# Optimization experiments

Hardware: AMD Instinct MI355X
Metric: run time of the kernel (lower is better)

The kernel has to match this reference:

```python
import jax, jax.numpy as jnp
import numpy as np
import math

D_MODEL = 1024
NUM_HEADS = 16
B, S = 4, 2048


def setup_inputs() -> dict:
    key = jax.random.key(0)
    ks = jax.random.split(key, 12)
    d = D_MODEL
    sc = 1.0 / math.sqrt(d)
    inp = {
        "q": jax.random.normal(ks[0], (B, S, d), jnp.float32),
        "k": jax.random.normal(ks[1], (B, S, d), jnp.float32),
        "v": jax.random.normal(ks[2], (B, S, d), jnp.float32),
        # causal mask, broadcast over batch and heads
        "mask": jnp.tril(jnp.ones((S, S), bool))[None, None, :, :],
        "Wq": jax.random.normal(ks[3], (d, d), jnp.float32) * sc,
        "bq": jnp.zeros((d,), jnp.float32),
        "Wk": jax.random.normal(ks[4], (d, d), jnp.float32) * sc,
        "bk": jnp.zeros((d,), jnp.float32),
        "Wv": jax.random.normal(ks[5], (d, d), jnp.float32) * sc,
        "bv": jnp.zeros((d,), jnp.float32),
        "Wo": jax.random.normal(ks[6], (d, d), jnp.float32) * sc,
        "bo": jnp.zeros((d,), jnp.float32),
    }
    return inp


def reference(q, k, v, mask, Wq, bq, Wk, bk, Wv, bv, Wo, bo):
    b, s, d = q.shape
    h = NUM_HEADS
    dk = d // h
    # QKV projections, then split heads: [B, H, S, dk]
    def split(x):
        return x.reshape(b, -1, h, dk).transpose(0, 2, 1, 3)
    Q = split(q @ Wq + bq)
    K = split(k @ Wk + bk)
    V = split(v @ Wv + bv)
    scores = jnp.einsum("bhqd,bhkd->bhqk", Q, K) / jnp.sqrt(jnp.float32(dk))
    scores = jnp.where(mask, scores, jnp.float32(-jnp.inf))
    attn = jax.nn.softmax(scores, axis=-1)  # dropout is identity in eval
    ctx = jnp.einsum("bhqk,bhkd->bhqd", attn, V)
    ctx = ctx.transpose(0, 2, 1, 3).reshape(b, -1, d)
    return ctx @ Wo + bo
```

## Files before the change

kernel.cpp:

```cpp
#include <hip/hip_runtime.h>
#include <hip/hip_bf16.h>

typedef unsigned short u16;
typedef __bf16 bf16x8 __attribute__((ext_vector_type(8)));
typedef float f32x4 __attribute__((ext_vector_type(4)));

#define D_MODEL 1024
#define NUM_HEADS 16
#define BATCH 4
#define SEQ 2048
#define DK 64
#define MROWS (BATCH * SEQ)
#define TENS (MROWS * D_MODEL)

#define GLOAD16(gp, lp) __builtin_amdgcn_global_load_lds( \
    (const __attribute__((address_space(1))) void*)(gp), \
    (__attribute__((address_space(3))) void*)(lp), 16, 0, 0)

__device__ inline u16 f2bf(float f) {
    __hip_bfloat16 h = __float2bfloat16(f);
    return *reinterpret_cast<u16*>(&h);
}

__global__ __launch_bounds__(256) void transpose4(
    const float* __restrict__ W0, const float* __restrict__ W1,
    const float* __restrict__ W2, const float* __restrict__ W3,
    u16* __restrict__ dst)
{
    __shared__ u16 tile[32][33];
    const float* in = (blockIdx.z == 0) ? W0 : (blockIdx.z == 1) ? W1
                    : (blockIdx.z == 2) ? W2 : W3;
    u16* out = dst + (size_t)blockIdx.z * (D_MODEL * D_MODEL);
    int x = blockIdx.x * 32 + threadIdx.x;
    int y = blockIdx.y * 32 + threadIdx.y;
    for (int i = 0; i < 32; i += 8)
        tile[threadIdx.y + i][threadIdx.x] = f2bf(in[(size_t)(y + i) * D_MODEL + x]);
    __syncthreads();
    x = blockIdx.y * 32 + threadIdx.x;
    y = blockIdx.x * 32 + threadIdx.y;
    for (int i = 0; i < 32; i += 8)
        out[(size_t)(y + i) * D_MODEL + x] = tile[threadIdx.x][threadIdx.y + i];
}

__global__ __launch_bounds__(256) void cvt_bf16(
    const float* __restrict__ x0, const float* __restrict__ x1,
    const float* __restrict__ x2,
    u16* __restrict__ o0, u16* __restrict__ o1, u16* __restrict__ o2)
{
    const int z = blockIdx.z;
    const float* x = (z == 0) ? x0 : (z == 1) ? x1 : x2;
    u16* o = (z == 0) ? o0 : (z == 1) ? o1 : o2;
    size_t i = ((size_t)blockIdx.x * 256 + threadIdx.x) * 8;
    f32x4 a = *(const f32x4*)(x + i);
    f32x4 b = *(const f32x4*)(x + i + 4);
    union { u16 s[8]; uint4 v; } u;
    for (int t = 0; t < 4; t++) { u.s[t] = f2bf(a[t]); u.s[4 + t] = f2bf(b[t]); }
    *(uint4*)(o + i) = u.v;
}

__global__ __launch_bounds__(256) void prep_fused(
    const float* __restrict__ q, const float* __restrict__ k,
    const float* __restrict__ v,
    u16* __restrict__ s0, u16* __restrict__ s1, u16* __restrict__ s2,
    const float* __restrict__ W0, const float* __restrict__ W1,
    const float* __restrict__ W2, const float* __restrict__ W3,
    u16* __restrict__ wt)
{
    __shared__ u16 tile[32][33];
    const int z = blockIdx.z;
    if (z < 3) {
        const float* x = (z == 0) ? q : (z == 1) ? k : v;
        u16* o = (z == 0) ? s0 : (z == 1) ? s1 : s2;
        size_t i = ((size_t)blockIdx.x * 256 + threadIdx.x) * 8;
        f32x4 a = *(const f32x4*)(x + i);
        f32x4 b = *(const f32x4*)(x + i + 4);
        union { u16 s[8]; uint4 v4; } u;
        for (int t = 0; t < 4; t++) { u.s[t] = f2bf(a[t]); u.s[4 + t] = f2bf(b[t]); }
        *(uint4*)(o + i) = u.v4;
    } else {
        const int bx = blockIdx.x & 31;
        const int by = (blockIdx.x >> 5) & 31;
        const int bz = blockIdx.x >> 10;
        const int tx = threadIdx.x & 31;
        const int ty = threadIdx.x >> 5;
        const float* in = (bz == 0) ? W0 : (bz == 1) ? W1
                        : (bz == 2) ? W2 : W3;
        u16* out = wt + (size_t)bz * (D_MODEL * D_MODEL);
        int x = bx * 32 + tx;
        int y = by * 32 + ty;
        for (int i = 0; i < 32; i += 8)
            tile[ty + i][tx] = f2bf(in[(size_t)(y + i) * D_MODEL + x]);
        __syncthreads();
        x = by * 32 + tx;
        y = bx * 32 + ty;
        for (int i = 0; i < 32; i += 8)
            out[(size_t)(y + i) * D_MODEL + x] = tile[tx][ty + i];
    }
}

template<bool C_F32>
__global__ __launch_bounds__(256) void gemm_b(
    const u16* __restrict__ A0, const u16* __restrict__ A1,
    const u16* __restrict__ A2,
    const u16* __restrict__ Bt0, const u16* __restrict__ Bt1,
    const u16* __restrict__ Bt2,
    const float* __restrict__ bias0, const float* __restrict__ bias1,
    const float* __restrict__ bias2,
    void* __restrict__ C0, void* __restrict__ C1, void* __restrict__ C2,
    float os0, float os1, float os2)
{
    const int z = blockIdx.z;
    const u16* A      = (z == 0) ? A0 : (z == 1) ? A1 : A2;
    const u16* Bt     = (z == 0) ? Bt0 : (z == 1) ? Bt1 : Bt2;
    const float* bias = (z == 0) ? bias0 : (z == 1) ? bias1 : bias2;
    void* Cp          = (z == 0) ? C0 : (z == 1) ? C1 : C2;
    const float os    = (z == 0) ? os0 : (z == 1) ? os1 : os2;
    const int K = D_MODEL, N = D_MODEL;

    __shared__ __align__(16) u16 As[128 * 32];
    __shared__ __align__(16) u16 Bs[128 * 32];

    const int tid  = threadIdx.x;
    const int lane = tid & 63;
    const int w    = tid >> 6;
    const int wr   = w >> 1, wc = w & 1;
    const int m0   = blockIdx.x * 128;
    const int n0   = blockIdx.y * 128;
    const int col_l = lane & 15;
    const int quad  = lane >> 4;
    const int koff  = quad * 8;

    const f32x4 fz = {0.f, 0.f, 0.f, 0.f};
    f32x4 acc[4][4];
    for (int i = 0; i < 4; i++)
        for (int j = 0; j < 4; j++) acc[i][j] = fz;

    for (int k0 = 0; k0 < K; k0 += 32) {
        __syncthreads();
        for (int i = 0; i < 2; i++) {
            int c   = w * 2 + i;
            int row = c * 16 + (lane >> 2);
            GLOAD16(A  + (size_t)(m0 + row) * K + k0 + (lane & 3) * 8, (char*)As + c * 1024);
            GLOAD16(Bt + (size_t)(n0 + row) * K + k0 + (lane & 3) * 8, (char*)Bs + c * 1024);
        }
        __syncthreads();

        bf16x8 af[4], bfr[4];
        for (int i = 0; i < 4; i++)
            af[i] = *(const bf16x8*)&As[(wr * 64 + i * 16 + col_l) * 32 + koff];
        for (int j = 0; j < 4; j++)
            bfr[j] = *(const bf16x8*)&Bs[(wc * 64 + j * 16 + col_l) * 32 + koff];
        for (int i = 0; i < 4; i++)
            for (int j = 0; j < 4; j++)
                acc[i][j] = __builtin_amdgcn_mfma_f32_16x16x32_bf16(
                    af[i], bfr[j], acc[i][j], 0, 0, 0);
    }

    const int row_q = quad * 4;
    for (int j = 0; j < 4; j++) {
        int colg = n0 + wc * 64 + j * 16 + col_l;
        float bv = bias[colg];
        for (int i = 0; i < 4; i++) {
            int rowg = m0 + wr * 64 + i * 16 + row_q;
            for (int r = 0; r < 4; r++) {
                float val = (acc[i][j][r] + bv) * os;
                if (C_F32)
                    ((float*)Cp)[(size_t)(rowg + r) * N + colg] = val;
                else
                    ((u16*)Cp)[(size_t)(rowg + r) * N + colg] = f2bf(val);
            }
        }
    }
}

__global__ __launch_bounds__(256) void attn_kernel(
    const u16* __restrict__ Q, const u16* __restrict__ K,
    const u16* __restrict__ V, u16* __restrict__ ctx)
{
    __shared__ __align__(16) u16 Ksf[64 * 64];
    __shared__ __align__(16) u16 Vts[64 * 64];
    __shared__ __align__(16) u16 Ps[4][16][72];

    const int tid  = threadIdx.x;
    const int lane = tid & 63;
    const int w    = tid >> 6;
    const int bh   = blockIdx.x;
    const int iy = blockIdx.y;
    const int sj = iy >> 2, jj4 = iy & 3;
    const int qt = (sj == 0) ? jj4 : (sj == 1) ? 15 - jj4
                 : (sj == 2) ? 7 - jj4 : 8 + jj4;
    const int b    = bh >> 4, h = bh & 15;
    const int q0   = qt * 128;
    const size_t rowbase = (size_t)b * SEQ;
    const int colbase = h * DK;

    const int col_l = lane & 15;
    const int quad  = lane >> 4;
    const int r0 = tid >> 3, cc0 = tid & 7, r1 = r0 + 32;

    const int c0 = w * 2, c1 = c0 + 1;
    const int krow0 = c0 * 8 + (lane >> 3), krow1 = c1 * 8 + (lane >> 3);
    const int bb0 = (lane & 7) ^ (krow0 & 7), bb1 = (lane & 7) ^ (krow1 & 7);
    const u16* Kg0 = K + (rowbase + krow0) * D_MODEL + colbase + bb0 * 8;
    const u16* Kg1 = K + (rowbase + krow1) * D_MODEL + colbase + bb1 * 8;
    u16* KsW0 = &Ksf[c0 * 512 + lane * 8];
    u16* KsW1 = &Ksf[c1 * 512 + lane * 8];
    const u16* Vg0 = V + (rowbase + r0) * D_MODEL + colbase + cc0 * 8;
    const u16* Vg1 = V + (rowbase + r1) * D_MODEL + colbase + cc0 * 8;

    bf16x8 aq[2][2];
    for (int rb = 0; rb < 2; rb++) {
        const u16* qp = Q + (rowbase + q0 + rb * 64 + w * 16 + col_l) * D_MODEL + colbase;
        aq[rb][0] = *(const bf16x8*)(qp + quad * 8);
        aq[rb][1] = *(const bf16x8*)(qp + 32 + quad * 8);
    }

    bf16x8 ones;
    for (int i = 0; i < 8; i++) ones[i] = (__bf16)1.0f;

    const f32x4 fz = {0.f, 0.f, 0.f, 0.f};
    f32x4 oacc[2][4];
    for (int rb = 0; rb < 2; rb++)
        for (int j = 0; j < 4; j++) oacc[rb][j] = fz;
    f32x4 lacc[2] = {fz, fz};

    const int ktmax = 2 * qt + 1;
    const size_t tstep = (size_t)64 * D_MODEL;

    uint4 kA0 = *(const uint4*)Kg0;
    uint4 kA1 = *(const uint4*)Kg1;
    uint4 vA0 = *(const uint4*)Vg0;
    uint4 vA1 = *(const uint4*)Vg1;

    for (int kt = 0; kt <= ktmax; kt++) {
        const int k0 = kt * 64;
        const size_t noff = (size_t)((kt < ktmax) ? kt + 1 : ktmax) * tstep;
        uint4 kB0 = *(const uint4*)(Kg0 + noff);
        uint4 kB1 = *(const uint4*)(Kg1 + noff);
        uint4 vB0 = *(const uint4*)(Vg0 + noff);
        uint4 vB1 = *(const uint4*)(Vg1 + noff);

        asm volatile("s_waitcnt lgkmcnt(0)" ::: "memory");
        __builtin_amdgcn_s_barrier();

        *(uint4*)KsW0 = kA0;
        *(uint4*)KsW1 = kA1;
        {
            union { uint4 v; u16 s[8]; } t0, t1;
            t0.v = vA0; t1.v = vA1;
            for (int jj = 0; jj < 8; jj++) {
                int fx = ((cc0 ^ jj) & 7) << 3;
                Vts[(cc0 * 8 + jj) * 64 + (r0 ^ fx)] = t0.s[jj];
                Vts[(cc0 * 8 + jj) * 64 + (r1 ^ fx)] = t1.s[jj];
            }
        }
        asm volatile("s_waitcnt lgkmcnt(0)" ::: "memory");
        __builtin_amdgcn_s_barrier();

        const bool rb0a = (kt <= 2 * qt);

        f32x4 s0acc[4], s1acc[4];
        for (int j = 0; j < 4; j++) { s0acc[j] = fz; s1acc[j] = fz; }
        __builtin_amdgcn_s_setprio(1);
        for (int j = 0; j < 4; j++) {
            int krow = j * 16 + col_l, sw = krow & 7;
            bf16x8 bk0 = *(const bf16x8*)&Ksf[krow * 64 + ((quad ^ sw) * 8)];
            bf16x8 bk1 = *(const bf16x8*)&Ksf[krow * 64 + (((4 + quad) ^ sw) * 8)];
            s0acc[j] = __builtin_amdgcn_mfma_f32_16x16x32_bf16(aq[0][0], bk0, s0acc[j], 0, 0, 0);
            s0acc[j] = __builtin_amdgcn_mfma_f32_16x16x32_bf16(aq[0][1], bk1, s0acc[j], 0, 0, 0);
            s1acc[j] = __builtin_amdgcn_mfma_f32_16x16x32_bf16(aq[1][0], bk0, s1acc[j], 0, 0, 0);
            s1acc[j] = __builtin_amdgcn_mfma_f32_16x16x32_bf16(aq[1][1], bk1, s1acc[j], 0, 0, 0);
        }
        __builtin_amdgcn_s_setprio(0);

        bf16x8 ap00, ap01, ap10, ap11;
        {
            const bool diag = (kt == 2 * qt);
            if (diag) {
                const int qg = q0 + w * 16 + quad * 4;
                for (int j = 0; j < 4; j++) {
                    int kg = k0 + j * 16 + col_l;
                    for (int r = 0; r < 4; r++) {
                        float e = __expf(s0acc[j][r]);
                        if (kg > qg + r) e = 0.f;
                        Ps[w][quad * 4 + r][j * 16 + col_l] = f2bf(e);
                    }
                }
            } else {
                for (int j = 0; j < 4; j++)
                    for (int r = 0; r < 4; r++)
                        Ps[w][quad * 4 + r][j * 16 + col_l] =
                            f2bf(__expf(s0acc[j][r]));
            }
            __threadfence_block();
            ap00 = *(const bf16x8*)&Ps[w][col_l][quad * 8];
            ap01 = *(const bf16x8*)&Ps[w][col_l][32 + quad * 8];
            if (rb0a) {
                lacc[0] = __builtin_amdgcn_mfma_f32_16x16x32_bf16(ap00, ones, lacc[0], 0, 0, 0);
                lacc[0] = __builtin_amdgcn_mfma_f32_16x16x32_bf16(ap01, ones, lacc[0], 0, 0, 0);
            }
        }
        __threadfence_block();
        {
            const bool diag = (kt == 2 * qt + 1);
            if (diag) {
                const int qg = q0 + 64 + w * 16 + quad * 4;
                for (int j = 0; j < 4; j++) {
                    int kg = k0 + j * 16 + col_l;
                    for (int r = 0; r < 4; r++) {
                        float e = __expf(s1acc[j][r]);
                        if (kg > qg + r) e = 0.f;
                        Ps[w][quad * 4 + r][j * 16 + col_l] = f2bf(e);
                    }
                }
            } else {
                for (int j = 0; j < 4; j++)
                    for (int r = 0; r < 4; r++)
                        Ps[w][quad * 4 + r][j * 16 + col_l] =
                            f2bf(__expf(s1acc[j][r]));
            }
            __threadfence_block();
            ap10 = *(const bf16x8*)&Ps[w][col_l][quad * 8];
            ap11 = *(const bf16x8*)&Ps[w][col_l][32 + quad * 8];
            lacc[1] = __builtin_amdgcn_mfma_f32_16x16x32_bf16(ap10, ones, lacc[1], 0, 0, 0);
            lacc[1] = __builtin_amdgcn_mfma_f32_16x16x32_bf16(ap11, ones, lacc[1], 0, 0, 0);
        }

        __builtin_amdgcn_s_setprio(1);
        for (int j = 0; j < 4; j++) {
            int vrow = j * 16 + col_l, sw = ((vrow >> 3) ^ vrow) & 7;
            bf16x8 bv0 = *(const bf16x8*)&Vts[vrow * 64 + ((quad ^ sw) * 8)];
            bf16x8 bv1 = *(const bf16x8*)&Vts[vrow * 64 + (((4 + quad) ^ sw) * 8)];
            if (rb0a) {
                oacc[0][j] = __builtin_amdgcn_mfma_f32_16x16x32_bf16(ap00, bv0, oacc[0][j], 0, 0, 0);
                oacc[0][j] = __builtin_amdgcn_mfma_f32_16x16x32_bf16(ap01, bv1, oacc[0][j], 0, 0, 0);
            }
            oacc[1][j] = __builtin_amdgcn_mfma_f32_16x16x32_bf16(ap10, bv0, oacc[1][j], 0, 0, 0);
            oacc[1][j] = __builtin_amdgcn_mfma_f32_16x16x32_bf16(ap11, bv1, oacc[1][j], 0, 0, 0);
        }
        __builtin_amdgcn_s_setprio(0);

        kA0 = kB0; kA1 = kB1; vA0 = vB0; vA1 = vB1;
    }

    for (int rb = 0; rb < 2; rb++) {
        for (int r = 0; r < 4; r++) {
            float inv = 1.f / lacc[rb][r];
            int rowg = q0 + rb * 64 + w * 16 + quad * 4 + r;
            for (int j = 0; j < 4; j++)
                ctx[(rowbase + rowg) * D_MODEL + colbase + j * 16 + col_l] =
                    f2bf(oacc[rb][j][r] * inv);
        }
    }
}

extern "C" void kernel_launch(void* const* d_in, const int* in_sizes, int n_in,
                              void* d_out, int out_size, void* d_ws, size_t ws_size,
                              hipStream_t stream) {
    const float* q  = (const float*)d_in[0];
    const float* k  = (const float*)d_in[1];
    const float* v  = (const float*)d_in[2];
    const float* Wq = (const float*)d_in[4];
    const float* bq = (const float*)d_in[5];
    const float* Wk = (const float*)d_in[6];
    const float* bk = (const float*)d_in[7];
    const float* Wv = (const float*)d_in[8];
    const float* bv = (const float*)d_in[9];
    const float* Wo = (const float*)d_in[10];
    const float* bo = (const float*)d_in[11];

    char* ws = (char*)d_ws;
    u16* Qb  = (u16*)(ws + (0ull  << 20));
    u16* Kb  = (u16*)(ws + (16ull << 20));
    u16* Vb  = (u16*)(ws + (32ull << 20));
    u16* WT  = (u16*)(ws + (48ull << 20));
    u16* WqT = WT + 0ull * D_MODEL * D_MODEL;
    u16* WkT = WT + 1ull * D_MODEL * D_MODEL;
    u16* WvT = WT + 2ull * D_MODEL * D_MODEL;
    u16* WoT = WT + 3ull * D_MODEL * D_MODEL;
    u16* ctx = Qb;
    u16* s0  = (u16*)d_out;
    u16* s1  = s0 + (size_t)TENS;

    const int cvt_blocks = TENS / (256 * 8);
    dim3 gg(MROWS / 128, D_MODEL / 128);

    const float qscale = 0.125f;

    const bool big_ws = (ws_size >= (73ull << 20));
    if (big_ws) {
        u16* s2 = (u16*)(ws + (56ull << 20));
        prep_fused<<<dim3(cvt_blocks, 1, 4), 256, 0, stream>>>(
            q, k, v, s0, s1, s2, Wq, Wk, Wv, Wo, WT);
        gemm_b<false><<<dim3(gg.x, gg.y, 3), 256, 0, stream>>>(
            s0, s1, s2, WqT, WkT, WvT, bq, bk, bv, Qb, Kb, Vb,
            qscale, 1.0f, 1.0f);
    } else {
        transpose4<<<dim3(32, 32, 4), dim3(32, 8), 0, stream>>>(Wq, Wk, Wv, Wo, WT);
        cvt_bf16<<<dim3(cvt_blocks, 1, 2), 256, 0, stream>>>(q, k, k, s0, s1, s1);
        gemm_b<false><<<dim3(gg.x, gg.y, 2), 256, 0, stream>>>(
            s0, s1, s1, WqT, WkT, WkT, bq, bk, bk, Qb, Kb, Kb,
            qscale, 1.0f, 1.0f);
        cvt_bf16<<<dim3(cvt_blocks, 1, 1), 256, 0, stream>>>(v, v, v, s0, s0, s0);
        gemm_b<false><<<dim3(gg.x, gg.y, 1), 256, 0, stream>>>(
            s0, s0, s0, WvT, WvT, WvT, bv, bv, bv, Vb, Vb, Vb,
            1.0f, 1.0f, 1.0f);
    }

    attn_kernel<<<dim3(BATCH * NUM_HEADS, SEQ / 128), 256, 0, stream>>>(Qb, Kb, Vb, ctx);

    gemm_b<true><<<dim3(gg.x, gg.y, 1), 256, 0, stream>>>(
        ctx, ctx, ctx, WoT, WoT, WoT, bo, bo, bo, d_out, d_out, d_out,
        1.0f, 1.0f, 1.0f);
}
```

Before: 324.6 us.

## Write V projection transposed from GEMM epilogue to simplify attention V staging

The V projection GEMM now writes its output transposed (feature-major, [d][B*S]) using packed 4-element stores, selected by a new ct_z argument. The attention kernel then loads V tiles already transposed and stores them to LDS with 16-byte vector writes, replacing the per-element scattered transpose into shared memory. This cuts LDS store instructions and bank conflicts in the attention inner loop. The cost is strided 8-byte global stores in the GEMM epilogue, which may coalesce less well than the original row-major writes.

```diff
diff --git a/kernel.cpp b/kernel.cpp
--- a/kernel.cpp
+++ b/kernel.cpp
@@ -107,7 +107,7 @@
     const float* __restrict__ bias0, const float* __restrict__ bias1,
     const float* __restrict__ bias2,
     void* __restrict__ C0, void* __restrict__ C1, void* __restrict__ C2,
-    float os0, float os1, float os2)
+    float os0, float os1, float os2, int ct_z)
 {
     const int z = blockIdx.z;
     const u16* A      = (z == 0) ? A0 : (z == 1) ? A1 : A2;
@@ -157,17 +157,25 @@
     }
 
     const int row_q = quad * 4;
+    const bool ct = (!C_F32) && (z == ct_z);
     for (int j = 0; j < 4; j++) {
         int colg = n0 + wc * 64 + j * 16 + col_l;
         float bv = bias[colg];
         for (int i = 0; i < 4; i++) {
             int rowg = m0 + wr * 64 + i * 16 + row_q;
-            for (int r = 0; r < 4; r++) {
-                float val = (acc[i][j][r] + bv) * os;
-                if (C_F32)
-                    ((float*)Cp)[(size_t)(rowg + r) * N + colg] = val;
-                else
-                    ((u16*)Cp)[(size_t)(rowg + r) * N + colg] = f2bf(val);
+            if (ct) {
+                union { u16 s[4]; uint2 v2; } pk;
+                for (int r = 0; r < 4; r++)
+                    pk.s[r] = f2bf((acc[i][j][r] + bv) * os);
+                *(uint2*)((u16*)Cp + (size_t)colg * MROWS + rowg) = pk.v2;
+            } else {
+                for (int r = 0; r < 4; r++) {
+                    float val = (acc[i][j][r] + bv) * os;
+                    if (C_F32)
+                        ((float*)Cp)[(size_t)(rowg + r) * N + colg] = val;
+                    else
+                        ((u16*)Cp)[(size_t)(rowg + r) * N + colg] = f2bf(val);
+                }
             }
         }
     }
@@ -175,7 +183,7 @@
 
 __global__ __launch_bounds__(256) void attn_kernel(
     const u16* __restrict__ Q, const u16* __restrict__ K,
-    const u16* __restrict__ V, u16* __restrict__ ctx)
+    const u16* __restrict__ Vt, u16* __restrict__ ctx)
 {
     __shared__ __align__(16) u16 Ksf[64 * 64];
     __shared__ __align__(16) u16 Vts[64 * 64];
@@ -196,7 +204,6 @@
 
     const int col_l = lane & 15;
     const int quad  = lane >> 4;
-    const int r0 = tid >> 3, cc0 = tid & 7, r1 = r0 + 32;
 
     const int c0 = w * 2, c1 = c0 + 1;
     const int krow0 = c0 * 8 + (lane >> 3), krow1 = c1 * 8 + (lane >> 3);
@@ -205,8 +212,13 @@
     const u16* Kg1 = K + (rowbase + krow1) * D_MODEL + colbase + bb1 * 8;
     u16* KsW0 = &Ksf[c0 * 512 + lane * 8];
     u16* KsW1 = &Ksf[c1 * 512 + lane * 8];
-    const u16* Vg0 = V + (rowbase + r0) * D_MODEL + colbase + cc0 * 8;
-    const u16* Vg1 = V + (rowbase + r1) * D_MODEL + colbase + cc0 * 8;
+    const int vd0 = krow0, vd1 = krow1;
+    const int bbv0 = (lane & 7) ^ ((c0 ^ (lane >> 3)) & 7);
+    const int bbv1 = (lane & 7) ^ ((c1 ^ (lane >> 3)) & 7);
+    const u16* Vg0 = Vt + (size_t)(colbase + vd0) * MROWS + rowbase + bbv0 * 8;
+    const u16* Vg1 = Vt + (size_t)(colbase + vd1) * MROWS + rowbase + bbv1 * 8;
+    u16* VsW0 = &Vts[c0 * 512 + lane * 8];
+    u16* VsW1 = &Vts[c1 * 512 + lane * 8];
 
     bf16x8 aq[2][2];
     for (int rb = 0; rb < 2; rb++) {
@@ -225,7 +237,7 @@
     f32x4 lacc[2] = {fz, fz};
 
     const int ktmax = 2 * qt + 1;
-    const size_t tstep = (size_t)64 * D_MODEL;
+    const size_t kstep = (size_t)64 * D_MODEL;
 
     uint4 kA0 = *(const uint4*)Kg0;
     uint4 kA1 = *(const uint4*)Kg1;
@@ -234,26 +246,21 @@
 
     for (int kt = 0; kt <= ktmax; kt++) {
         const int k0 = kt * 64;
-        const size_t noff = (size_t)((kt < ktmax) ? kt + 1 : ktmax) * tstep;
-        uint4 kB0 = *(const uint4*)(Kg0 + noff);
-        uint4 kB1 = *(const uint4*)(Kg1 + noff);
-        uint4 vB0 = *(const uint4*)(Vg0 + noff);
-        uint4 vB1 = *(const uint4*)(Vg1 + noff);
+        const int ktn = (kt < ktmax) ? kt + 1 : ktmax;
+        const size_t noffK = (size_t)ktn * kstep;
+        const size_t noffV = (size_t)ktn * 64;
+        uint4 kB0 = *(const uint4*)(Kg0 + noffK);
+        uint4 kB1 = *(const uint4*)(Kg1 + noffK);
+        uint4 vB0 = *(const uint4*)(Vg0 + noffV);
+        uint4 vB1 = *(const uint4*)(Vg1 + noffV);
 
         asm volatile("s_waitcnt lgkmcnt(0)" ::: "memory");
         __builtin_amdgcn_s_barrier();
 
         *(uint4*)KsW0 = kA0;
         *(uint4*)KsW1 = kA1;
-        {
-            union { uint4 v; u16 s[8]; } t0, t1;
-            t0.v = vA0; t1.v = vA1;
-            for (int jj = 0; jj < 8; jj++) {
-                int fx = ((cc0 ^ jj) & 7) << 3;
-                Vts[(cc0 * 8 + jj) * 64 + (r0 ^ fx)] = t0.s[jj];
-                Vts[(cc0 * 8 + jj) * 64 + (r1 ^ fx)] = t1.s[jj];
-            }
-        }
+        *(uint4*)VsW0 = vA0;
+        *(uint4*)VsW1 = vA1;
         asm volatile("s_waitcnt lgkmcnt(0)" ::: "memory");
         __builtin_amdgcn_s_barrier();
 
@@ -372,7 +379,7 @@
     char* ws = (char*)d_ws;
     u16* Qb  = (u16*)(ws + (0ull  << 20));
     u16* Kb  = (u16*)(ws + (16ull << 20));
-    u16* Vb  = (u16*)(ws + (32ull << 20));
+    u16* Vt  = (u16*)(ws + (32ull << 20));
     u16* WT  = (u16*)(ws + (48ull << 20));
     u16* WqT = WT + 0ull * D_MODEL * D_MODEL;
     u16* WkT = WT + 1ull * D_MODEL * D_MODEL;
@@ -393,23 +400,23 @@
         prep_fused<<<dim3(cvt_blocks, 1, 4), 256, 0, stream>>>(
             q, k, v, s0, s1, s2, Wq, Wk, Wv, Wo, WT);
         gemm_b<false><<<dim3(gg.x, gg.y, 3), 256, 0, stream>>>(
-            s0, s1, s2, WqT, WkT, WvT, bq, bk, bv, Qb, Kb, Vb,
-            qscale, 1.0f, 1.0f);
+            s0, s1, s2, WqT, WkT, WvT, bq, bk, bv, Qb, Kb, Vt,
+            qscale, 1.0f, 1.0f, 2);
     } else {
         transpose4<<<dim3(32, 32, 4), dim3(32, 8), 0, stream>>>(Wq, Wk, Wv, Wo, WT);
         cvt_bf16<<<dim3(cvt_blocks, 1, 2), 256, 0, stream>>>(q, k, k, s0, s1, s1);
         gemm_b<false><<<dim3(gg.x, gg.y, 2), 256, 0, stream>>>(
             s0, s1, s1, WqT, WkT, WkT, bq, bk, bk, Qb, Kb, Kb,
-            qscale, 1.0f, 1.0f);
+            qscale, 1.0f, 1.0f, -1);
         cvt_bf16<<<dim3(cvt_blocks, 1, 1), 256, 0, stream>>>(v, v, v, s0, s0, s0);
         gemm_b<false><<<dim3(gg.x, gg.y, 1), 256, 0, stream>>>(
-            s0, s0, s0, WvT, WvT, WvT, bv, bv, bv, Vb, Vb, Vb,
-            1.0f, 1.0f, 1.0f);
-    }
-
-    attn_kernel<<<dim3(BATCH * NUM_HEADS, SEQ / 128), 256, 0, stream>>>(Qb, Kb, Vb, ctx);
+            s0, s0, s0, WvT, WvT, WvT, bv, bv, bv, Vt, Vt, Vt,
+            1.0f, 1.0f, 1.0f, 0);
+    }
+
+    attn_kernel<<<dim3(BATCH * NUM_HEADS, SEQ / 128), 256, 0, stream>>>(Qb, Kb, Vt, ctx);
 
     gemm_b<true><<<dim3(gg.x, gg.y, 1), 256, 0, stream>>>(
         ctx, ctx, ctx, WoT, WoT, WoT, bo, bo, bo, d_out, d_out, d_out,
-        1.0f, 1.0f, 1.0f);
-}
+        1.0f, 1.0f, 1.0f, -1);
+}
```

Result: slower. 338.2 us (+4.2%).
